# Performance work log

Measured on AMD Instinct MI355X. Metric: run time of the kernel, lower is better.

## Reference

```python
import jax, jax.numpy as jnp
import numpy as np

BATCH, LENGTH, INPUT, HIDDEN = 64, 2048, 128, 256

def setup_inputs() -> dict:
    key = jax.random.key(0)
    k1, k2, k3, k4 = jax.random.split(key, 4)
    x = jax.random.normal(k1, (BATCH, LENGTH, INPUT), dtype=jnp.float32)
    h = jnp.zeros((BATCH, HIDDEN), dtype=jnp.float32)
    W_x = jax.random.normal(k2, (HIDDEN, INPUT), dtype=jnp.float32)
    W_h = jax.random.normal(k3, (HIDDEN, HIDDEN), dtype=jnp.float32)
    b_h = jax.random.normal(k4, (HIDDEN,), dtype=jnp.float32)
    return {"x": x, "h": h, "W_x": W_x, "W_h": W_h, "b_h": b_h}

def reference(x, h, W_x, W_h, b_h):
    # x: [b, l, i]; h: [b, hidden]; returns [l, b, hidden] (matches torch forward)
    # Pre-compute input projection for all timesteps in one GEMM: [b, l, hidden]
    xw = jnp.einsum('bli,hi->blh', x, W_x)
    xw_t = jnp.swapaxes(xw, 0, 1)  # [l, b, hidden]

    def step(h, xw_step):
        h_new = jnp.tanh(xw_step + h @ W_h.T + b_h)
        return h_new, h_new

    _, output = jax.lax.scan(step, h, xw_t)
    return output  # [l, b, hidden]
```

## Files before the change

### kernel.cpp

```cpp
#include <hip/hip_runtime.h>

#define BATCH 64
#define LEN   2048
#define NIN   128
#define NH    256

typedef float f32x4 __attribute__((ext_vector_type(4)));
typedef float f32x2 __attribute__((ext_vector_type(2)));

__device__ __forceinline__ float tanh_xla_fma_f32(float x) {
  const float kClamp = 7.99881172180175781f;
  float xc = fmaxf(x, -kClamp);
  xc = fminf(xc, kClamp);
  float x2 = xc * xc;
  float num = fmaf(x2, -2.76076847742355e-16f, 2.00018790482477e-13f);
  num = fmaf(x2, num, -8.60467152213735e-11f);
  num = fmaf(x2, num, 5.12229709037114e-08f);
  num = fmaf(x2, num, 1.48572235717979e-05f);
  num = fmaf(x2, num, 6.37261928875436e-04f);
  num = fmaf(x2, num, 4.89352455891786e-03f);
  num = xc * num;
  float den = fmaf(x2, 1.19825839466702e-06f, 1.18534705686654e-04f);
  den = fmaf(x2, den, 2.26843463243900e-03f);
  den = fmaf(x2, den, 4.89352518554385e-03f);
  float r = num / den;
  return (fabsf(x) < 0.0004f) ? x : r;
}

#define PINV(v) asm("" : "+v"(v));

#define RLANE(val, q) \
  __uint_as_float(__builtin_amdgcn_readlane(__float_as_uint(val), (q)))

#define REPQ48(M) M(0) M(1) M(2) M(3) M(4) M(5) M(6) M(7) \
  M(8) M(9) M(10) M(11) M(12) M(13) M(14) M(15) \
  M(16) M(17) M(18) M(19) M(20) M(21) M(22) M(23) \
  M(24) M(25) M(26) M(27) M(28) M(29) M(30) M(31) \
  M(32) M(33) M(34) M(35) M(36) M(37) M(38) M(39) \
  M(40) M(41) M(42) M(43) M(44) M(45) M(46) M(47)
#define REPQ16(M) M(48) M(49) M(50) M(51) M(52) M(53) M(54) M(55) \
  M(56) M(57) M(58) M(59) M(60) M(61) M(62) M(63)
#define REPX32(M) M(0) M(1) M(2) M(3) M(4) M(5) M(6) M(7) \
  M(8) M(9) M(10) M(11) M(12) M(13) M(14) M(15) \
  M(16) M(17) M(18) M(19) M(20) M(21) M(22) M(23) \
  M(24) M(25) M(26) M(27) M(28) M(29) M(30) M(31)

#define WQ_DECL(n) f32x4 wq##n;
#define WQ_LOAD(n) wq##n = wrow[n]; PINV(wq##n)
#define AQ_DECL(n) float aq##n##x, aq##n##y, aq##n##z, aq##n##w;
#define AQ_LOAD(n) { f32x4 v = wrow[n]; \
  asm("v_accvgpr_write_b32 %0, %1" : "=a"(aq##n##x) : "v"(v.x)); \
  asm("v_accvgpr_write_b32 %0, %1" : "=a"(aq##n##y) : "v"(v.y)); \
  asm("v_accvgpr_write_b32 %0, %1" : "=a"(aq##n##z) : "v"(v.z)); \
  asm("v_accvgpr_write_b32 %0, %1" : "=a"(aq##n##w) : "v"(v.w)); }

#define STEPV(n) \
  acc = fmaf(RLANE(hq.x, n), wq##n.x, acc); \
  acc = fmaf(RLANE(hq.y, n), wq##n.y, acc); \
  acc = fmaf(RLANE(hq.z, n), wq##n.z, acc); \
  acc = fmaf(RLANE(hq.w, n), wq##n.w, acc);
#define STEPA(n) { float t0, t1, t2, t3; \
  asm volatile("v_accvgpr_read_b32 %0, %1" : "=v"(t0) : "a"(aq##n##x)); \
  asm volatile("v_accvgpr_read_b32 %0, %1" : "=v"(t1) : "a"(aq##n##y)); \
  asm volatile("v_accvgpr_read_b32 %0, %1" : "=v"(t2) : "a"(aq##n##z)); \
  asm volatile("v_accvgpr_read_b32 %0, %1" : "=v"(t3) : "a"(aq##n##w)); \
  acc = fmaf(RLANE(hq.x, n), t0, acc); \
  acc = fmaf(RLANE(hq.y, n), t1, acc); \
  acc = fmaf(RLANE(hq.z, n), t2, acc); \
  acc = fmaf(RLANE(hq.w, n), t3, acc); }

#define XSTEP(n) \
  acc = fmaf(RLANE(xv.x, 2*(n)    ), wq##n.x, acc); \
  acc = fmaf(RLANE(xv.y, 2*(n)    ), wq##n.y, acc); \
  acc = fmaf(RLANE(xv.x, 2*(n) + 1), wq##n.z, acc); \
  acc = fmaf(RLANE(xv.y, 2*(n) + 1), wq##n.w, acc);

constexpr int LC = 128;

__global__ __launch_bounds__(256, 2)
void xw_kernel(const float* __restrict__ x, const float* __restrict__ Wx,
               float* __restrict__ out) {
  const int j    = threadIdx.x;
  const int lane = j & 63;
  const int b    = blockIdx.x & (BATCH - 1);
  const int lt   = blockIdx.x >> 6;

  const f32x4* wrow = (const f32x4*)&Wx[(size_t)j * NIN];
  REPX32(WQ_DECL)
  REPX32(WQ_LOAD)

  const float* xr = x + ((size_t)b * LEN + (size_t)lt * LC) * NIN;
  float* op = out + ((size_t)lt * LC * BATCH + b) * NH + j;

  f32x2 xv = *(const f32x2*)(xr + 2 * lane);
  for (int ll = 0; ll < LC; ++ll) {
    const int ln = (ll + 1 < LC) ? (ll + 1) : ll;
    f32x2 xnext = *(const f32x2*)(xr + (size_t)ln * NIN + 2 * lane);
    float acc = 0.0f;
    REPX32(XSTEP)
    op[(size_t)ll * BATCH * NH] = acc;
    xv = xnext;
  }
}

__global__ __launch_bounds__(256)
__attribute__((amdgpu_waves_per_eu(1, 1)))
void rnn_kernel(const float* __restrict__ Wh, const float* __restrict__ bh,
                const float* __restrict__ h0, float* __restrict__ io) {
  const int b    = blockIdx.x;
  const int j    = threadIdx.x;
  const int lane = j & 63;

  __shared__ __align__(16) float hbuf[2][NH];

  const f32x4* wrow = (const f32x4*)&Wh[(size_t)j * NH];
  REPQ48(WQ_DECL)
  REPQ16(AQ_DECL)
  REPQ48(WQ_LOAD)
  REPQ16(AQ_LOAD)

  const float bias = bh[j];
  hbuf[0][j] = h0[b * NH + j];
  __syncthreads();

  float* p = io + (size_t)b * NH + j;
  const size_t stride = (size_t)BATCH * NH;

  float xw = p[0];
  int cur = 0;

  for (int l = 0; l < LEN; ++l) {
    const int ln = (l + 1 < LEN) ? (l + 1) : l;
    const float xw_next = p[(size_t)ln * stride];

    const f32x4 hq = *(const f32x4*)&hbuf[cur][4 * lane];
    float acc = 0.0f;
    REPQ48(STEPV)
    REPQ16(STEPA)

    float pre;
    {
#pragma clang fp contract(off)
      pre = (xw + acc) + bias;
    }
    const float hn = tanh_xla_fma_f32(pre);

    p[(size_t)l * stride] = hn;
    hbuf[cur ^ 1][j] = hn;

    asm volatile("s_waitcnt lgkmcnt(0)" ::: "memory");
    __builtin_amdgcn_s_barrier();
    asm volatile("" ::: "memory");

    cur ^= 1;
    xw = xw_next;
  }
}

extern "C" void kernel_launch(void* const* d_in, const int* in_sizes, int n_in,
                              void* d_out, int out_size, void* d_ws, size_t ws_size,
                              hipStream_t stream) {
  const float* x  = (const float*)d_in[0];
  const float* h0 = (const float*)d_in[1];
  const float* Wx = (const float*)d_in[2];
  const float* Wh = (const float*)d_in[3];
  const float* bh = (const float*)d_in[4];
  for (int i = 0; i < n_in; ++i) {
    switch (in_sizes[i]) {
      case 16777216: x  = (const float*)d_in[i]; break;
      case 16384:    h0 = (const float*)d_in[i]; break;
      case 32768:    Wx = (const float*)d_in[i]; break;
      case 65536:    Wh = (const float*)d_in[i]; break;
      case 256:      bh = (const float*)d_in[i]; break;
      default: break;
    }
  }
  float* out = (float*)d_out;

  xw_kernel<<<dim3((LEN / LC) * BATCH), dim3(256), 0, stream>>>(x, Wx, out);
  rnn_kernel<<<dim3(BATCH), dim3(256), 0, stream>>>(Wh, bh, h0, out);
}
```

Baseline: 2.623 ms.

## Keep all weights in AGPRs and software-pipeline readlane/accvgpr reads in inline asm

Moves all recurrent and input-projection weights into accumulation registers and replaces the compiler-scheduled dot product with hand-written inline assembly. The assembly double-buffers the accvgpr reads and v_readlane broadcasts of the next chunk while the FMAs of the current chunk run. The aim is to hide readlane and accvgpr-read latency on the serial recurrence critical path and to free VGPRs. The risks are extra accvgpr_read instructions per step, which were previously avoided for 48 of the 64 quads, and readlane-to-SGPR hazards that need wait states.

Result: slower. 3.841 ms (+46.4%).

```diff
diff --git a/kernel.cpp b/kernel.cpp
--- a/kernel.cpp
+++ b/kernel.cpp
@@ -27,26 +27,20 @@
   return (fabsf(x) < 0.0004f) ? x : r;
 }
 
-#define PINV(v) asm("" : "+v"(v));
-
-#define RLANE(val, q) \
-  __uint_as_float(__builtin_amdgcn_readlane(__float_as_uint(val), (q)))
-
-#define REPQ48(M) M(0) M(1) M(2) M(3) M(4) M(5) M(6) M(7) \
+
+#define REP64(M) M(0) M(1) M(2) M(3) M(4) M(5) M(6) M(7) \
   M(8) M(9) M(10) M(11) M(12) M(13) M(14) M(15) \
   M(16) M(17) M(18) M(19) M(20) M(21) M(22) M(23) \
   M(24) M(25) M(26) M(27) M(28) M(29) M(30) M(31) \
   M(32) M(33) M(34) M(35) M(36) M(37) M(38) M(39) \
-  M(40) M(41) M(42) M(43) M(44) M(45) M(46) M(47)
-#define REPQ16(M) M(48) M(49) M(50) M(51) M(52) M(53) M(54) M(55) \
+  M(40) M(41) M(42) M(43) M(44) M(45) M(46) M(47) \
+  M(48) M(49) M(50) M(51) M(52) M(53) M(54) M(55) \
   M(56) M(57) M(58) M(59) M(60) M(61) M(62) M(63)
-#define REPX32(M) M(0) M(1) M(2) M(3) M(4) M(5) M(6) M(7) \
+#define REP32(M) M(0) M(1) M(2) M(3) M(4) M(5) M(6) M(7) \
   M(8) M(9) M(10) M(11) M(12) M(13) M(14) M(15) \
   M(16) M(17) M(18) M(19) M(20) M(21) M(22) M(23) \
   M(24) M(25) M(26) M(27) M(28) M(29) M(30) M(31)
 
-#define WQ_DECL(n) f32x4 wq##n;
-#define WQ_LOAD(n) wq##n = wrow[n]; PINV(wq##n)
 #define AQ_DECL(n) float aq##n##x, aq##n##y, aq##n##z, aq##n##w;
 #define AQ_LOAD(n) { f32x4 v = wrow[n]; \
   asm("v_accvgpr_write_b32 %0, %1" : "=a"(aq##n##x) : "v"(v.x)); \
@@ -54,26 +48,87 @@
   asm("v_accvgpr_write_b32 %0, %1" : "=a"(aq##n##z) : "v"(v.z)); \
   asm("v_accvgpr_write_b32 %0, %1" : "=a"(aq##n##w) : "v"(v.w)); }
 
-#define STEPV(n) \
-  acc = fmaf(RLANE(hq.x, n), wq##n.x, acc); \
-  acc = fmaf(RLANE(hq.y, n), wq##n.y, acc); \
-  acc = fmaf(RLANE(hq.z, n), wq##n.z, acc); \
-  acc = fmaf(RLANE(hq.w, n), wq##n.w, acc);
-#define STEPA(n) { float t0, t1, t2, t3; \
-  asm volatile("v_accvgpr_read_b32 %0, %1" : "=v"(t0) : "a"(aq##n##x)); \
-  asm volatile("v_accvgpr_read_b32 %0, %1" : "=v"(t1) : "a"(aq##n##y)); \
-  asm volatile("v_accvgpr_read_b32 %0, %1" : "=v"(t2) : "a"(aq##n##z)); \
-  asm volatile("v_accvgpr_read_b32 %0, %1" : "=v"(t3) : "a"(aq##n##w)); \
-  acc = fmaf(RLANE(hq.x, n), t0, acc); \
-  acc = fmaf(RLANE(hq.y, n), t1, acc); \
-  acc = fmaf(RLANE(hq.z, n), t2, acc); \
-  acc = fmaf(RLANE(hq.w, n), t3, acc); }
-
-#define XSTEP(n) \
-  acc = fmaf(RLANE(xv.x, 2*(n)    ), wq##n.x, acc); \
-  acc = fmaf(RLANE(xv.y, 2*(n)    ), wq##n.y, acc); \
-  acc = fmaf(RLANE(xv.x, 2*(n) + 1), wq##n.z, acc); \
-  acc = fmaf(RLANE(xv.y, 2*(n) + 1), wq##n.w, acc);
+#define BANKS float w0A,w1A,w2A,w3A,w0B,w1B,w2B,w3B; \
+              float s0A,s1A,s2A,s3A,s0B,s1B,s2B,s3B;
+
+#define QLD(B) asm volatile( \
+  "v_accvgpr_read_b32 %[w0], %[ax]\n\t" \
+  "v_readlane_b32 %[s0], %[hx], 0\n\t" \
+  "v_accvgpr_read_b32 %[w1], %[ay]\n\t" \
+  "v_readlane_b32 %[s1], %[hy], 0\n\t" \
+  "v_accvgpr_read_b32 %[w2], %[az]\n\t" \
+  "v_readlane_b32 %[s2], %[hz], 0\n\t" \
+  "v_accvgpr_read_b32 %[w3], %[aw]\n\t" \
+  "v_readlane_b32 %[s3], %[hw], 0" \
+  : [w0]"=&v"(w0##B), [w1]"=&v"(w1##B), [w2]"=&v"(w2##B), [w3]"=&v"(w3##B), \
+    [s0]"=&s"(s0##B), [s1]"=&s"(s1##B), [s2]"=&s"(s2##B), [s3]"=&s"(s3##B) \
+  : [ax]"a"(aq0x), [ay]"a"(aq0y), [az]"a"(aq0z), [aw]"a"(aq0w), \
+    [hx]"v"(hq.x), [hy]"v"(hq.y), [hz]"v"(hq.z), [hw]"v"(hq.w));
+
+#define QS(n, np, CB, NB) asm volatile( \
+  "v_accvgpr_read_b32 %[nw0], %[ax]\n\t" \
+  "v_readlane_b32 %[ns0], %[hx], %[ln]\n\t" \
+  "v_fma_f32 %[a], %[cs0], %[cw0], %[a]\n\t" \
+  "v_accvgpr_read_b32 %[nw1], %[ay]\n\t" \
+  "v_readlane_b32 %[ns1], %[hy], %[ln]\n\t" \
+  "v_fma_f32 %[a], %[cs1], %[cw1], %[a]\n\t" \
+  "v_accvgpr_read_b32 %[nw2], %[az]\n\t" \
+  "v_readlane_b32 %[ns2], %[hz], %[ln]\n\t" \
+  "v_fma_f32 %[a], %[cs2], %[cw2], %[a]\n\t" \
+  "v_accvgpr_read_b32 %[nw3], %[aw]\n\t" \
+  "v_readlane_b32 %[ns3], %[hw], %[ln]\n\t" \
+  "v_fma_f32 %[a], %[cs3], %[cw3], %[a]" \
+  : [a]"+v"(acc), \
+    [nw0]"=&v"(w0##NB), [nw1]"=&v"(w1##NB), [nw2]"=&v"(w2##NB), [nw3]"=&v"(w3##NB), \
+    [ns0]"=&s"(s0##NB), [ns1]"=&s"(s1##NB), [ns2]"=&s"(s2##NB), [ns3]"=&s"(s3##NB) \
+  : [cw0]"v"(w0##CB), [cw1]"v"(w1##CB), [cw2]"v"(w2##CB), [cw3]"v"(w3##CB), \
+    [cs0]"s"(s0##CB), [cs1]"s"(s1##CB), [cs2]"s"(s2##CB), [cs3]"s"(s3##CB), \
+    [ax]"a"(aq##np##x), [ay]"a"(aq##np##y), [az]"a"(aq##np##z), [aw]"a"(aq##np##w), \
+    [hx]"v"(hq.x), [hy]"v"(hq.y), [hz]"v"(hq.z), [hw]"v"(hq.w), [ln]"i"(np));
+
+#define QF(CB) asm volatile( \
+  "v_fma_f32 %[a], %[cs0], %[cw0], %[a]\n\t" \
+  "v_fma_f32 %[a], %[cs1], %[cw1], %[a]\n\t" \
+  "v_fma_f32 %[a], %[cs2], %[cw2], %[a]\n\t" \
+  "v_fma_f32 %[a], %[cs3], %[cw3], %[a]" \
+  : [a]"+v"(acc) \
+  : [cw0]"v"(w0##CB), [cw1]"v"(w1##CB), [cw2]"v"(w2##CB), [cw3]"v"(w3##CB), \
+    [cs0]"s"(s0##CB), [cs1]"s"(s1##CB), [cs2]"s"(s2##CB), [cs3]"s"(s3##CB));
+
+#define XLD(B) asm volatile( \
+  "v_accvgpr_read_b32 %[w0], %[ax]\n\t" \
+  "v_readlane_b32 %[s0], %[vx], 0\n\t" \
+  "v_accvgpr_read_b32 %[w1], %[ay]\n\t" \
+  "v_readlane_b32 %[s1], %[vy], 0\n\t" \
+  "v_accvgpr_read_b32 %[w2], %[az]\n\t" \
+  "v_readlane_b32 %[s2], %[vx], 1\n\t" \
+  "v_accvgpr_read_b32 %[w3], %[aw]\n\t" \
+  "v_readlane_b32 %[s3], %[vy], 1" \
+  : [w0]"=&v"(w0##B), [w1]"=&v"(w1##B), [w2]"=&v"(w2##B), [w3]"=&v"(w3##B), \
+    [s0]"=&s"(s0##B), [s1]"=&s"(s1##B), [s2]"=&s"(s2##B), [s3]"=&s"(s3##B) \
+  : [ax]"a"(aq0x), [ay]"a"(aq0y), [az]"a"(aq0z), [aw]"a"(aq0w), \
+    [vx]"v"(xv.x), [vy]"v"(xv.y));
+
+#define XS(n, np, CB, NB) asm volatile( \
+  "v_accvgpr_read_b32 %[nw0], %[ax]\n\t" \
+  "v_readlane_b32 %[ns0], %[vx], %[l0]\n\t" \
+  "v_fma_f32 %[a], %[cs0], %[cw0], %[a]\n\t" \
+  "v_accvgpr_read_b32 %[nw1], %[ay]\n\t" \
+  "v_readlane_b32 %[ns1], %[vy], %[l0]\n\t" \
+  "v_fma_f32 %[a], %[cs1], %[cw1], %[a]\n\t" \
+  "v_accvgpr_read_b32 %[nw2], %[az]\n\t" \
+  "v_readlane_b32 %[ns2], %[vx], %[l1]\n\t" \
+  "v_fma_f32 %[a], %[cs2], %[cw2], %[a]\n\t" \
+  "v_accvgpr_read_b32 %[nw3], %[aw]\n\t" \
+  "v_readlane_b32 %[ns3], %[vy], %[l1]\n\t" \
+  "v_fma_f32 %[a], %[cs3], %[cw3], %[a]" \
+  : [a]"+v"(acc), \
+    [nw0]"=&v"(w0##NB), [nw1]"=&v"(w1##NB), [nw2]"=&v"(w2##NB), [nw3]"=&v"(w3##NB), \
+    [ns0]"=&s"(s0##NB), [ns1]"=&s"(s1##NB), [ns2]"=&s"(s2##NB), [ns3]"=&s"(s3##NB) \
+  : [cw0]"v"(w0##CB), [cw1]"v"(w1##CB), [cw2]"v"(w2##CB), [cw3]"v"(w3##CB), \
+    [cs0]"s"(s0##CB), [cs1]"s"(s1##CB), [cs2]"s"(s2##CB), [cs3]"s"(s3##CB), \
+    [ax]"a"(aq##np##x), [ay]"a"(aq##np##y), [az]"a"(aq##np##z), [aw]"a"(aq##np##w), \
+    [vx]"v"(xv.x), [vy]"v"(xv.y), [l0]"i"(2*(np)), [l1]"i"(2*(np)+1));
 
 constexpr int LC = 128;
 
@@ -86,8 +141,9 @@
   const int lt   = blockIdx.x >> 6;
 
   const f32x4* wrow = (const f32x4*)&Wx[(size_t)j * NIN];
-  REPX32(WQ_DECL)
-  REPX32(WQ_LOAD)
+  REP32(AQ_DECL)
+  REP32(AQ_LOAD)
+  BANKS
 
   const float* xr = x + ((size_t)b * LEN + (size_t)lt * LC) * NIN;
   float* op = out + ((size_t)lt * LC * BATCH + b) * NH + j;
@@ -97,7 +153,16 @@
     const int ln = (ll + 1 < LC) ? (ll + 1) : ll;
     f32x2 xnext = *(const f32x2*)(xr + (size_t)ln * NIN + 2 * lane);
     float acc = 0.0f;
-    REPX32(XSTEP)
+    XLD(A)
+    XS(0,1,A,B)   XS(1,2,B,A)   XS(2,3,A,B)   XS(3,4,B,A)
+    XS(4,5,A,B)   XS(5,6,B,A)   XS(6,7,A,B)   XS(7,8,B,A)
+    XS(8,9,A,B)   XS(9,10,B,A)  XS(10,11,A,B) XS(11,12,B,A)
+    XS(12,13,A,B) XS(13,14,B,A) XS(14,15,A,B) XS(15,16,B,A)
+    XS(16,17,A,B) XS(17,18,B,A) XS(18,19,A,B) XS(19,20,B,A)
+    XS(20,21,A,B) XS(21,22,B,A) XS(22,23,A,B) XS(23,24,B,A)
+    XS(24,25,A,B) XS(25,26,B,A) XS(26,27,A,B) XS(27,28,B,A)
+    XS(28,29,A,B) XS(29,30,B,A) XS(30,31,A,B)
+    QF(B)
     op[(size_t)ll * BATCH * NH] = acc;
     xv = xnext;
   }
@@ -114,10 +179,9 @@
   __shared__ __align__(16) float hbuf[2][NH];
 
   const f32x4* wrow = (const f32x4*)&Wh[(size_t)j * NH];
-  REPQ48(WQ_DECL)
-  REPQ16(AQ_DECL)
-  REPQ48(WQ_LOAD)
-  REPQ16(AQ_LOAD)
+  REP64(AQ_DECL)
+  REP64(AQ_LOAD)
+  BANKS
 
   const float bias = bh[j];
   hbuf[0][j] = h0[b * NH + j];
@@ -135,8 +199,24 @@
 
     const f32x4 hq = *(const f32x4*)&hbuf[cur][4 * lane];
     float acc = 0.0f;
-    REPQ48(STEPV)
-    REPQ16(STEPA)
+    QLD(A)
+    QS(0,1,A,B)   QS(1,2,B,A)   QS(2,3,A,B)   QS(3,4,B,A)
+    QS(4,5,A,B)   QS(5,6,B,A)   QS(6,7,A,B)   QS(7,8,B,A)
+    QS(8,9,A,B)   QS(9,10,B,A)  QS(10,11,A,B) QS(11,12,B,A)
+    QS(12,13,A,B) QS(13,14,B,A) QS(14,15,A,B) QS(15,16,B,A)
+    QS(16,17,A,B) QS(17,18,B,A) QS(18,19,A,B) QS(19,20,B,A)
+    QS(20,21,A,B) QS(21,22,B,A) QS(22,23,A,B) QS(23,24,B,A)
+    QS(24,25,A,B) QS(25,26,B,A) QS(26,27,A,B) QS(27,28,B,A)
+    QS(28,29,A,B) QS(29,30,B,A) QS(30,31,A,B) QS(31,32,B,A)
+    QS(32,33,A,B) QS(33,34,B,A) QS(34,35,A,B) QS(35,36,B,A)
+    QS(36,37,A,B) QS(37,38,B,A) QS(38,39,A,B) QS(39,40,B,A)
+    QS(40,41,A,B) QS(41,42,B,A) QS(42,43,A,B) QS(43,44,B,A)
+    QS(44,45,A,B) QS(45,46,B,A) QS(46,47,A,B) QS(47,48,B,A)
+    QS(48,49,A,B) QS(49,50,B,A) QS(50,51,A,B) QS(51,52,B,A)
+    QS(52,53,A,B) QS(53,54,B,A) QS(54,55,A,B) QS(55,56,B,A)
+    QS(56,57,A,B) QS(57,58,B,A) QS(58,59,A,B) QS(59,60,B,A)
+    QS(60,61,A,B) QS(61,62,B,A) QS(62,63,A,B)
+    QF(B)
 
     float pre;
     {
```
